# Kernel tuning notes

Measured on AMD Instinct MI355X. Metric: run time of the kernel, lower is better.

Reference implementation:

```python
import jax, jax.numpy as jnp
import numpy as np

VOCAB = 20
HID = 128
ACT = 3
IN_DIM = VOCAB + 3
NUM_GRAPHS = 64
N_P, E_P = 100000, 1600000
N_M, E_M = 50000, 800000


def _gcn_conv(x, src, dst, W, b, n_nodes):
    deg = jax.ops.segment_sum(jnp.ones(src.shape[0], x.dtype), dst, num_segments=n_nodes) + 1.0
    dinv = jax.lax.rsqrt(deg)
    xw = x @ W                                    # [N, out]
    coef = dinv[src] * dinv[dst]                  # [E]
    agg = jax.ops.segment_sum(xw[src] * coef[:, None], dst, num_segments=n_nodes)
    # self-loop contribution: norm = dinv[i]*dinv[i] = 1/deg[i]
    return agg + xw / deg[:, None] + b


def _mean_pool(x, batch, n_graphs):
    s = jax.ops.segment_sum(x, batch, num_segments=n_graphs)
    cnt = jax.ops.segment_sum(jnp.ones(x.shape[0], x.dtype), batch, num_segments=n_graphs)
    return s / jnp.maximum(cnt, 1.0)[:, None]


def setup_inputs() -> dict:
    key = jax.random.key(0)
    ks = jax.random.split(key, 24)
    d = {}
    d['residue_p'] = jax.random.randint(ks[0], (N_P,), 0, VOCAB)
    d['pos_p'] = jax.random.normal(ks[1], (N_P, 3), jnp.float32)
    d['edge_index_p'] = jax.random.randint(ks[2], (2, E_P), 0, N_P)
    d['batch_p'] = jnp.sort(jax.random.randint(ks[3], (N_P,), 0, NUM_GRAPHS))
    d['residue_m'] = jax.random.randint(ks[4], (N_M,), 0, VOCAB)
    d['pos_m'] = jax.random.normal(ks[5], (N_M, 3), jnp.float32)
    d['edge_index_m'] = jax.random.randint(ks[6], (2, E_M), 0, N_M)
    d['batch_m'] = jnp.sort(jax.random.randint(ks[7], (N_M,), 0, NUM_GRAPHS))
    s = 0.05
    d['W_p1'] = jax.random.normal(ks[8], (IN_DIM, HID), jnp.float32) * s
    d['b_p1'] = jnp.zeros((HID,), jnp.float32)
    d['W_p2'] = jax.random.normal(ks[9], (HID, HID), jnp.float32) * s
    d['b_p2'] = jnp.zeros((HID,), jnp.float32)
    d['W_m1'] = jax.random.normal(ks[10], (IN_DIM, HID), jnp.float32) * s
    d['b_m1'] = jnp.zeros((HID,), jnp.float32)
    d['W_m2'] = jax.random.normal(ks[11], (HID, HID), jnp.float32) * s
    d['b_m2'] = jnp.zeros((HID,), jnp.float32)
    d['W1'] = jax.random.normal(ks[12], (2 * HID, HID), jnp.float32) * s
    d['b1'] = jnp.zeros((HID,), jnp.float32)
    d['W2'] = jax.random.normal(ks[13], (HID, ACT), jnp.float32) * s
    d['b2'] = jnp.zeros((ACT,), jnp.float32)
    return d


def reference(residue_p, pos_p, edge_index_p, batch_p,
              residue_m, pos_m, edge_index_m, batch_m,
              W_p1, b_p1, W_p2, b_p2, W_m1, b_m1, W_m2, b_m2,
              W1, b1, W2, b2):
    # protein branch
    x_p = jnp.concatenate([jax.nn.one_hot(residue_p, VOCAB, dtype=jnp.float32), pos_p], axis=1)
    sp, dp = edge_index_p[0], edge_index_p[1]
    x_p = jax.nn.relu(_gcn_conv(x_p, sp, dp, W_p1, b_p1, N_P))
    x_p = jax.nn.relu(_gcn_conv(x_p, sp, dp, W_p2, b_p2, N_P))
    protein_embedding = _mean_pool(x_p, batch_p, NUM_GRAPHS)  # [G, HID]
    # micromolecule branch
    x_m = jnp.concatenate([jax.nn.one_hot(residue_m, VOCAB, dtype=jnp.float32), pos_m], axis=1)
    sm, dm = edge_index_m[0], edge_index_m[1]
    x_m = jax.nn.relu(_gcn_conv(x_m, sm, dm, W_m1, b_m1, N_M))
    x_m = jax.nn.relu(_gcn_conv(x_m, sm, dm, W_m2, b_m2, N_M))
    # inject protein context per micromolecule node
    ctx = protein_embedding[batch_m]                # [N_M, HID]
    feat = jnp.concatenate([x_m, ctx], axis=1)      # [N_M, 2*HID]
    h = jax.nn.relu(feat @ W1 + b1)
    return h @ W2 + b2                              # [N_M, ACT]
```

## Files before the change

kernel.cpp:

```cpp
#include <hip/hip_runtime.h>
#include <hip/hip_bf16.h>
#include <hip/hip_fp16.h>

#define HID 128
#define BIN_T 8192
#define NBMAX 1664
#define CAP 2560

typedef _Float16 f16;
typedef __attribute__((ext_vector_type(2))) _Float16 f16x2;
typedef __attribute__((ext_vector_type(4))) _Float16 f16x4;
typedef __attribute__((ext_vector_type(8))) _Float16 f16x8;
typedef __attribute__((ext_vector_type(4))) float f32x4;



__global__ void k_prep_all(const float* __restrict__ Wp2, const float* __restrict__ Wm2,
                           const float* __restrict__ W1,
                           f16* __restrict__ Wp2t, f16* __restrict__ Wm2t,
                           f16* __restrict__ W1at,
                           int* __restrict__ bcur_p, int* __restrict__ bcur_m,
                           const int* __restrict__ batch_p, int* __restrict__ pcnt,
                           float* __restrict__ psum, int N_P) {
    int idx = blockIdx.x * 256 + threadIdx.x;
    if (idx < 16384) {
        int n = idx & 127, k = idx >> 7;
        Wp2t[n * 128 + k] = (f16)Wp2[k * 128 + n];
        Wm2t[n * 128 + k] = (f16)Wm2[k * 128 + n];
        W1at[n * 128 + k] = (f16)W1[k * 128 + n];
    }
    if (idx <= NBMAX) { bcur_p[idx] = idx * CAP; bcur_m[idx] = idx * CAP; }
    if (idx < 64 * HID) psum[idx] = 0.f;
    if (idx < 64) {
        int g = idx;
        int lo = 0, hi = N_P;
        while (lo < hi) { int mid = (lo + hi) >> 1; if (batch_p[mid] < g) lo = mid + 1; else hi = mid; }
        int a = lo;
        lo = 0; hi = N_P;
        while (lo < hi) { int mid = (lo + hi) >> 1; if (batch_p[mid] < g + 1) lo = mid + 1; else hi = mid; }
        pcnt[g] = lo - a;
    }
}


__global__ void k_tile_bin2(const int* __restrict__ src_p, const int* __restrict__ dst_p,
                            int* __restrict__ bcur_p, unsigned int* __restrict__ pairs_p,
                            int E_p, int NB_p, int TP,
                            const int* __restrict__ src_m, const int* __restrict__ dst_m,
                            int* __restrict__ bcur_m, unsigned int* __restrict__ pairs_m,
                            int E_m, int NB_m) {
    __shared__ unsigned int dbuf[BIN_T];
    __shared__ unsigned short perm[BIN_T];
    __shared__ int hist[NBMAX];
    __shared__ int lbase[NBMAX];
    __shared__ int gbase[NBMAX];
    __shared__ int tt[256];
    bool isP = (int)blockIdx.x < TP;
    const int* src = isP ? src_p : src_m;
    const int* dst = isP ? dst_p : dst_m;
    int* bcursor = isP ? bcur_p : bcur_m;
    unsigned int* pairs = isP ? pairs_p : pairs_m;
    int E = isP ? E_p : E_m;
    int NB = isP ? NB_p : NB_m;
    int tilebase = (isP ? blockIdx.x : blockIdx.x - TP) * BIN_T;
    int t = threadIdx.x;
    int n = min(BIN_T, E - tilebase);
    for (int i = t; i < NB; i += 256) hist[i] = 0;
    __syncthreads();
    for (int i = t; i < n; i += 256) {
        unsigned int d = (unsigned int)dst[tilebase + i];
        dbuf[i] = d;
        atomicAdd(&hist[d >> 6], 1);
    }
    __syncthreads();
    {
        int b0 = t * 7, loc[7], run = 0;
        #pragma unroll
        for (int k = 0; k < 7; ++k) {
            int b = b0 + k;
            int c = (b < NB) ? hist[b] : 0;
            loc[k] = run; run += c;
        }
        tt[t] = run;
        __syncthreads();
        int val = run;
        for (int off = 1; off < 256; off <<= 1) {
            int add = (t >= off) ? tt[t - off] : 0;
            __syncthreads();
            tt[t] += add;
            __syncthreads();
        }
        int ebase = tt[t] - val;
        #pragma unroll
        for (int k = 0; k < 7; ++k) {
            int b = b0 + k;
            if (b < NB) lbase[b] = ebase + loc[k];
        }
    }
    __syncthreads();
    for (int i = t; i < NB; i += 256) {
        int c = hist[i];
        gbase[i] = (c > 0) ? atomicAdd(&bcursor[i], c) : 0;
    }
    __syncthreads();
    for (int i = t; i < NB; i += 256) hist[i] = lbase[i];
    __syncthreads();
    for (int i = t; i < n; i += 256) {
        int b = (int)(dbuf[i] >> 6);
        int p = atomicAdd(&hist[b], 1);
        perm[p] = (unsigned short)i;
    }
    __syncthreads();
    for (int p = t; p < n; p += 256) {
        int li = perm[p];
        unsigned int d = dbuf[li];
        int b = (int)(d >> 6);
        int addr = gbase[b] + (p - lbase[b]);
        pairs[addr] = (unsigned int)src[tilebase + li] | ((d & 63u) << 26);
    }
}


__global__ void k_fill_a(
        const unsigned int* __restrict__ pairs_p, const int* __restrict__ bcur_p,
        const int* __restrict__ res_p, const float* __restrict__ pos_p,
        int4* __restrict__ rec16_p, float* __restrict__ dinv_p,
        int* __restrict__ rowptr_p, int* __restrict__ rowend_p, int* __restrict__ csr_p,
        int N_p, int NB_p,
        const unsigned int* __restrict__ pairs_m, const int* __restrict__ bcur_m,
        const int* __restrict__ res_m, const float* __restrict__ pos_m,
        int4* __restrict__ rec16_m, float* __restrict__ dinv_m,
        int* __restrict__ rowptr_m, int* __restrict__ rowend_m, int* __restrict__ csr_m,
        int N_m) {
    __shared__ int cnt[64];
    __shared__ int cur[64];
    bool isP = (int)blockIdx.x < NB_p;
    const unsigned int* pairs = isP ? pairs_p : pairs_m;
    const int* bcur = isP ? bcur_p : bcur_m;
    const int* residue = isP ? res_p : res_m;
    const float* pos = isP ? pos_p : pos_m;
    int4* rec16 = isP ? rec16_p : rec16_m;
    float* dinvA = isP ? dinv_p : dinv_m;
    int* rowptr = isP ? rowptr_p : rowptr_m;
    int* rowend = isP ? rowend_p : rowend_m;
    int* csr_src = isP ? csr_p : csr_m;
    int N = isP ? N_p : N_m;
    int b = isP ? blockIdx.x : blockIdx.x - NB_p;
    int t = threadIdx.x, base = b * 64;
    if (t < 64) cnt[t] = 0;
    __syncthreads();
    int lo = b * CAP, hi = bcur[b];
    for (int e = lo + t; e < hi; e += 256)
        atomicAdd(&cnt[pairs[e] >> 26], 1);
    __syncthreads();
    if (t < 64) {
        int off = 0;
        for (int k = 0; k < t; ++k) off += cnt[k];
        int node = base + t;
        if (node < N) {
            rowptr[node] = lo + off;
            rowend[node] = lo + off + cnt[t];
            float d = (float)cnt[t] + 1.0f;
            float di = 1.0f / sqrtf(d);
            dinvA[node] = di;
            float px = pos[node * 3 + 0], py = pos[node * 3 + 1], pz = pos[node * 3 + 2];
            f16x4 r;
            r[0] = (f16)di; r[1] = (f16)(di * px); r[2] = (f16)(di * py); r[3] = (f16)(di * pz);
            int4 rc;
            rc.x = ((const int*)&r)[0];
            rc.y = ((const int*)&r)[1];
            rc.z = residue[node];
            rc.w = 0;
            rec16[node] = rc;
        }
        cur[t] = lo + off;
    }
    __syncthreads();
    for (int e = lo + t; e < hi; e += 256) {
        unsigned int pk = pairs[e];
        int slot = atomicAdd(&cur[pk >> 26], 1);
        csr_src[slot] = (int)(pk & 0x1FFFFu);
    }
}


__global__ __launch_bounds__(256) void k_l1(
        const unsigned int* __restrict__ pairs_p, const int* __restrict__ bcur_p,
        const int4* __restrict__ rec16_p,
        const float* __restrict__ W_p, const float* __restrict__ bias_p,
        const float* __restrict__ dinv_p, f16* __restrict__ y1_p, int N_p, int NB_p,
        const unsigned int* __restrict__ pairs_m, const int* __restrict__ bcur_m,
        const int4* __restrict__ rec16_m,
        const float* __restrict__ W_m, const float* __restrict__ bias_m,
        const float* __restrict__ dinv_m, f16* __restrict__ y1_m, int N_m) {
    __shared__ float acc[64][25];
    __shared__ float sdv[64];
    bool isP = (int)blockIdx.x < NB_p;
    const unsigned int* pairs = isP ? pairs_p : pairs_m;
    const int* bcur = isP ? bcur_p : bcur_m;
    const int4* rec16 = isP ? rec16_p : rec16_m;
    const float* W = isP ? W_p : W_m;
    const float* bias = isP ? bias_p : bias_m;
    const float* dinvA = isP ? dinv_p : dinv_m;
    f16* y1h = isP ? y1_p : y1_m;
    int N = isP ? N_p : N_m;
    int b = isP ? blockIdx.x : blockIdx.x - NB_p;
    int t = threadIdx.x, base = b * 64;
    for (int q = t; q < 64 * 25; q += 256) ((float*)acc)[q] = 0.f;
    if (t < 64 && base + t < N) sdv[t] = dinvA[base + t];
    int jj = (t & 63) * 2, slot = t >> 6;
    float wreg[23][2];
    #pragma unroll
    for (int k = 0; k < 23; ++k) {
        float2 wv = *(const float2*)&W[k * 128 + jj];
        wreg[k][0] = wv.x; wreg[k][1] = wv.y;
    }
    __syncthreads();
    int lo = b * CAP, hi = bcur[b];
    for (int e = lo + t; e < hi; e += 1024) {
        unsigned int pk[4];
        int4 rc[4];
        bool hv[4];
        #pragma unroll
        for (int u = 0; u < 4; ++u) {
            int ee = e + u * 256;
            hv[u] = ee < hi;
            pk[u] = pairs[hv[u] ? ee : e];
        }
        #pragma unroll
        for (int u = 0; u < 4; ++u)
            rc[u] = rec16[pk[u] & 0x1FFFFu];
        #pragma unroll
        for (int u = 0; u < 4; ++u) {
            if (!hv[u]) continue;
            f16x2 lo2 = *(const f16x2*)&rc[u].x;
            f16x2 hi2 = *(const f16x2*)&rc[u].y;
            int dl = (int)(pk[u] >> 26);
            int rs = rc[u].z;
            atomicAdd(&acc[dl][rs], (float)lo2[0]);
            atomicAdd(&acc[dl][20], (float)lo2[1]);
            atomicAdd(&acc[dl][21], (float)hi2[0]);
            atomicAdd(&acc[dl][22], (float)hi2[1]);
        }
    }
    __syncthreads();
    if (t < 64) {
        int node = base + t;
        if (node < N) {
            int4 rc = rec16[node];
            f16x2 lo2 = *(const f16x2*)&rc.x;
            f16x2 hi2 = *(const f16x2*)&rc.y;
            acc[t][rc.z] += (float)lo2[0];
            acc[t][20] += (float)lo2[1];
            acc[t][21] += (float)hi2[0];
            acc[t][22] += (float)hi2[1];
            float di = sdv[t];
            #pragma unroll
            for (int k = 0; k < 23; ++k) acc[t][k] *= di;
        }
    }
    __syncthreads();
    float bj0 = bias[jj], bj1 = bias[jj + 1];
    for (int r = slot * 16; r < slot * 16 + 16; ++r) {
        int node = base + r;
        if (node >= N) break;
        float a0 = bj0, a1 = bj1;
        #pragma unroll
        for (int k = 0; k < 23; ++k) {
            float zv = acc[r][k];
            a0 += zv * wreg[k][0];
            a1 += zv * wreg[k][1];
        }
        float dv = sdv[r];
        f16x2 o;
        o[0] = (f16)(fmaxf(a0, 0.f) * dv);
        o[1] = (f16)(fmaxf(a1, 0.f) * dv);
        *(f16x2*)&y1h[(size_t)node * HID + jj] = o;
    }
}


#define AGG16_TO_LDS(zs, y1h, rowptr, rowend, csr_src, dinvA, N)                \
    {                                                                           \
        const __half2* y2 = (const __half2*)y1h;                                \
        for (int i = 0; i < 4; ++i) {                                           \
            int node = tile + w * 4 + i;                                        \
            int cn = min(node, N - 1);                                          \
            int s0 = rowptr[cn], s1 = rowend[cn];                               \
            float ax = 0.f, ay = 0.f;                                           \
            int e = s0;                                                         \
            for (; e + 8 <= s1; e += 8) {                                       \
                float2 v0 = __half22float2(y2[(size_t)csr_src[e] * 64 + lane]);     \
                float2 v1 = __half22float2(y2[(size_t)csr_src[e + 1] * 64 + lane]); \
                float2 v2 = __half22float2(y2[(size_t)csr_src[e + 2] * 64 + lane]); \
                float2 v3 = __half22float2(y2[(size_t)csr_src[e + 3] * 64 + lane]); \
                float2 v4 = __half22float2(y2[(size_t)csr_src[e + 4] * 64 + lane]); \
                float2 v5 = __half22float2(y2[(size_t)csr_src[e + 5] * 64 + lane]); \
                float2 v6 = __half22float2(y2[(size_t)csr_src[e + 6] * 64 + lane]); \
                float2 v7 = __half22float2(y2[(size_t)csr_src[e + 7] * 64 + lane]); \
                ax += (v0.x + v1.x) + (v2.x + v3.x) + (v4.x + v5.x) + (v6.x + v7.x); \
                ay += (v0.y + v1.y) + (v2.y + v3.y) + (v4.y + v5.y) + (v6.y + v7.y); \
            }                                                                   \
            for (; e + 4 <= s1; e += 4) {                                       \
                float2 v0 = __half22float2(y2[(size_t)csr_src[e] * 64 + lane]);     \
                float2 v1 = __half22float2(y2[(size_t)csr_src[e + 1] * 64 + lane]); \
                float2 v2 = __half22float2(y2[(size_t)csr_src[e + 2] * 64 + lane]); \
                float2 v3 = __half22float2(y2[(size_t)csr_src[e + 3] * 64 + lane]); \
                ax += (v0.x + v1.x) + (v2.x + v3.x);                            \
                ay += (v0.y + v1.y) + (v2.y + v3.y);                            \
            }                                                                   \
            for (; e < s1; ++e) {                                               \
                float2 v = __half22float2(y2[(size_t)csr_src[e] * 64 + lane]);  \
                ax += v.x; ay += v.y;                                           \
            }                                                                   \
            float di = dinvA[cn];                                               \
            float2 vs = __half22float2(y2[(size_t)cn * 64 + lane]);             \
            f16x2 o;                                                            \
            o[0] = (f16)((ax + vs.x) * di);                                     \
            o[1] = (f16)((ay + vs.y) * di);                                     \
            *(f16x2*)&zs[w * 4 + i][lane * 2] = o;                              \
        }                                                                       \
    }                                                                           \
    __syncthreads();


__global__ __launch_bounds__(256) void k_agg_combined(
        const f16* __restrict__ y1p, const int* __restrict__ rpp, const int* __restrict__ rep,
        const int* __restrict__ csrp, const float* __restrict__ dvp,
        const f16* __restrict__ Wp2t, const float* __restrict__ bp2,
        const int* __restrict__ batchp, float* __restrict__ psum, int Np, int PB,
        const f16* __restrict__ y1m, const int* __restrict__ rpm, const int* __restrict__ rem,
        const int* __restrict__ csrm, const float* __restrict__ dvm,
        const f16* __restrict__ Wm2t, const float* __restrict__ bm2,
        f16* __restrict__ x2g, int Nm) {
    __shared__ f16 zs[16][136];
    int t = threadIdx.x, lane = t & 63, w = t >> 6;
    int lr = lane & 15, kb = lane >> 4;
    bool isP = (int)blockIdx.x < PB;
    if (isP) {
        const f16* y1h = y1p;
        int N = Np;
        int tile = blockIdx.x * 16;
        AGG16_TO_LDS(zs, y1h, rpp, rep, csrp, dvp, N)
        int g0 = batchp[min(tile, N - 1)];
        bool uni = (tile + 15 < N) && (g0 == batchp[tile + 15]);
        int gr[4]; bool val[4];
        if (!uni) {
            #pragma unroll
            for (int r = 0; r < 4; ++r) {
                int row = tile + kb * 4 + r;
                val[r] = row < N;
                gr[r] = batchp[min(row, N - 1)];
            }
        }
        f16x8 afr[4];
        #pragma unroll
        for (int kc = 0; kc < 4; ++kc)
            afr[kc] = *(const f16x8*)&zs[lr][kc * 32 + kb * 8];
        #pragma unroll
        for (int q = 0; q < 2; ++q) {
            int ct = w * 2 + q;
            f32x4 c4 = {0.f, 0.f, 0.f, 0.f};
            int col = ct * 16 + lr;
            const f16* wp = Wp2t + (size_t)col * HID + kb * 8;
            #pragma unroll
            for (int kc = 0; kc < 4; ++kc) {
                f16x8 bf = *(const f16x8*)(wp + kc * 32);
                c4 = __builtin_amdgcn_mfma_f32_16x16x32_f16(afr[kc], bf, c4, 0, 0, 0);
            }
            float bj = bp2[col];
            if (uni) {
                float ps = 0.f;
                #pragma unroll
                for (int r = 0; r < 4; ++r) ps += fmaxf(c4[r] + bj, 0.f);
                ps += __shfl_xor(ps, 16);
                ps += __shfl_xor(ps, 32);
                if (kb == 0) atomicAdd(&psum[g0 * HID + col], ps);
            } else {
                #pragma unroll
                for (int r = 0; r < 4; ++r)
                    if (val[r]) atomicAdd(&psum[gr[r] * HID + col], fmaxf(c4[r] + bj, 0.f));
            }
        }
    } else {
        const f16* y1h = y1m;
        int N = Nm;
        int tile = (blockIdx.x - PB) * 16;
        AGG16_TO_LDS(zs, y1h, rpm, rem, csrm, dvm, N)
        f16x8 afr[4];
        #pragma unroll
        for (int kc = 0; kc < 4; ++kc)
            afr[kc] = *(const f16x8*)&zs[lr][kc * 32 + kb * 8];
        __syncthreads();
        #pragma unroll
        for (int q = 0; q < 2; ++q) {
            int ct = w * 2 + q;
            f32x4 c4 = {0.f, 0.f, 0.f, 0.f};
            int col = ct * 16 + lr;
            const f16* wp = Wm2t + (size_t)col * HID + kb * 8;
            #pragma unroll
            for (int kc = 0; kc < 4; ++kc) {
                f16x8 bf = *(const f16x8*)(wp + kc * 32);
                c4 = __builtin_amdgcn_mfma_f32_16x16x32_f16(afr[kc], bf, c4, 0, 0, 0);
            }
            float bj = bm2[col];
            #pragma unroll
            for (int r = 0; r < 4; ++r)
                zs[kb * 4 + r][col] = (f16)fmaxf(c4[r] + bj, 0.f);
        }
        __syncthreads();
        int row = t >> 4, c8 = (t & 15) * 8;
        if (tile + row < N)
            *(f16x8*)&x2g[(size_t)(tile + row) * HID + c8] = *(const f16x8*)&zs[row][c8];
    }
}

__global__ void k_ctxw_div(const float* __restrict__ psum, const int* __restrict__ pcnt,
                           const float* __restrict__ W1, const float* __restrict__ b1,
                           float* __restrict__ ctxW) {
    __shared__ float pr[128];
    int g = blockIdx.x, j = threadIdx.x;
    pr[j] = psum[g * HID + j] / fmaxf((float)pcnt[g], 1.f);
    __syncthreads();
    float a = b1[j];
    #pragma unroll 4
    for (int k = 0; k < HID; ++k) a += pr[k] * W1[(HID + k) * HID + j];
    ctxW[g * HID + j] = a;
}

__global__ __launch_bounds__(256) void k_mm_finish(
        const f16* __restrict__ x2g, const int* __restrict__ batch,
        const float* __restrict__ ctxW, const f16* __restrict__ W1at,
        const float* __restrict__ W2, const float* __restrict__ b2,
        float* __restrict__ out, int N) {
    __shared__ float part[4][16][3];
    int tile = blockIdx.x * 16;
    int t = threadIdx.x, lane = t & 63, w = t >> 6;
    int lr = lane & 15, kb = lane >> 4;
    int cr = min(tile + lr, N - 1);
    f16x8 afr[4];
    #pragma unroll
    for (int kc = 0; kc < 4; ++kc)
        afr[kc] = *(const f16x8*)&x2g[(size_t)cr * HID + kc * 32 + kb * 8];
    int gidx[4];
    #pragma unroll
    for (int r = 0; r < 4; ++r)
        gidx[r] = batch[min(tile + kb * 4 + r, N - 1)];
    float po[4][3] = {};
    #pragma unroll
    for (int q = 0; q < 2; ++q) {
        int ct = w * 2 + q;
        f32x4 c4 = {0.f, 0.f, 0.f, 0.f};
        int col = ct * 16 + lr;
        const f16* wp = W1at + (size_t)col * HID + kb * 8;
        #pragma unroll
        for (int kc = 0; kc < 4; ++kc) {
            f16x8 bf = *(const f16x8*)(wp + kc * 32);
            c4 = __builtin_amdgcn_mfma_f32_16x16x32_f16(afr[kc], bf, c4, 0, 0, 0);
        }
        float w0 = W2[col * 3 + 0], w1 = W2[col * 3 + 1], w2 = W2[col * 3 + 2];
        #pragma unroll
        for (int r = 0; r < 4; ++r) {
            float h = fmaxf(c4[r] + ctxW[gidx[r] * HID + col], 0.f);
            po[r][0] += h * w0;
            po[r][1] += h * w1;
            po[r][2] += h * w2;
        }
    }
    #pragma unroll
    for (int m = 1; m < 16; m <<= 1) {
        #pragma unroll
        for (int r = 0; r < 4; ++r) {
            po[r][0] += __shfl_xor(po[r][0], m);
            po[r][1] += __shfl_xor(po[r][1], m);
            po[r][2] += __shfl_xor(po[r][2], m);
        }
    }
    if (lr == 0) {
        #pragma unroll
        for (int r = 0; r < 4; ++r) {
            part[w][kb * 4 + r][0] = po[r][0];
            part[w][kb * 4 + r][1] = po[r][1];
            part[w][kb * 4 + r][2] = po[r][2];
        }
    }
    __syncthreads();
    if (t < 48) {
        int row = t / 3, c = t - row * 3;
        int gr2 = tile + row;
        if (gr2 < N)
            out[(size_t)gr2 * 3 + c] = part[0][row][c] + part[1][row][c] +
                                       part[2][row][c] + part[3][row][c] + b2[c];
    }
}


extern "C" void kernel_launch(void* const* d_in, const int* in_sizes, int n_in,
                              void* d_out, int out_size, void* d_ws, size_t ws_size,
                              hipStream_t stream) {
    const int*   residue_p = (const int*)d_in[0];
    const float* pos_p     = (const float*)d_in[1];
    const int*   ei_p      = (const int*)d_in[2];
    const int*   batch_p   = (const int*)d_in[3];
    const int*   residue_m = (const int*)d_in[4];
    const float* pos_m     = (const float*)d_in[5];
    const int*   ei_m      = (const int*)d_in[6];
    const int*   batch_m   = (const int*)d_in[7];
    const float* W_p1 = (const float*)d_in[8];
    const float* b_p1 = (const float*)d_in[9];
    const float* W_p2 = (const float*)d_in[10];
    const float* b_p2 = (const float*)d_in[11];
    const float* W_m1 = (const float*)d_in[12];
    const float* b_m1 = (const float*)d_in[13];
    const float* W_m2 = (const float*)d_in[14];
    const float* b_m2 = (const float*)d_in[15];
    const float* W1   = (const float*)d_in[16];
    const float* b1   = (const float*)d_in[17];
    const float* W2   = (const float*)d_in[18];
    const float* b2   = (const float*)d_in[19];

    const int N_P = in_sizes[0];
    const int E_P = in_sizes[2] / 2;
    const int N_M = in_sizes[4];
    const int E_M = in_sizes[6] / 2;
    const int G = 64;
    const int NB_P = (N_P + 63) / 64;
    const int NB_M = (N_M + 63) / 64;
    const int PB = (N_P + 15) / 16;
    const int MB = (N_M + 15) / 16;

    char* ws = (char*)d_ws;
    size_t off = 0;
    auto alloc = [&](size_t bytes) {
        char* p = ws + off;
        off += (bytes + 511) & ~size_t(511);
        return p;
    };
    f16*           y1_p    = (f16*)  alloc((size_t)N_P * HID * 2);
    f16*           y1_m    = (f16*)  alloc((size_t)N_M * HID * 2);
    f16*           x2g     = (f16*)  alloc((size_t)N_M * HID * 2);
    int4*          rec16_p = (int4*) alloc((size_t)N_P * 16);
    int4*          rec16_m = (int4*) alloc((size_t)N_M * 16);
    float*         dinv_p  = (float*)alloc((size_t)N_P * 4);
    float*         dinv_m  = (float*)alloc((size_t)N_M * 4);
    int*           rp_p    = (int*)  alloc((size_t)N_P * 4);
    int*           rp_m    = (int*)  alloc((size_t)N_M * 4);
    int*           re_p    = (int*)  alloc((size_t)N_P * 4);
    int*           re_m    = (int*)  alloc((size_t)N_M * 4);
    int*           bcur_p  = (int*)  alloc((NBMAX + 1) * 4);
    int*           bcur_m  = (int*)  alloc((NBMAX + 1) * 4);
    unsigned int*  prs_p   = (unsigned int*)alloc((size_t)NB_P * CAP * 4);
    unsigned int*  prs_m   = (unsigned int*)alloc((size_t)NB_M * CAP * 4);
    int*           csr_p   = (int*)  alloc((size_t)NB_P * CAP * 4);
    int*           csr_m   = (int*)  alloc((size_t)NB_M * CAP * 4);
    float*         psum    = (float*)alloc((size_t)G * HID * 4);
    int*           pcnt    = (int*)  alloc((size_t)G * 4);
    float*         ctxW    = (float*)alloc((size_t)G * HID * 4);
    f16*           Wp2t    = (f16*)  alloc(128 * 128 * 2);
    f16*           Wm2t    = (f16*)  alloc(128 * 128 * 2);
    f16*           W1at    = (f16*)  alloc(128 * 128 * 2);

    const int TP = (E_P + BIN_T - 1) / BIN_T;
    const int TM = (E_M + BIN_T - 1) / BIN_T;

    k_prep_all<<<64, 256, 0, stream>>>(W_p2, W_m2, W1, Wp2t, Wm2t, W1at,
                                       bcur_p, bcur_m, batch_p, pcnt, psum, N_P);
    k_tile_bin2<<<TP + TM, 256, 0, stream>>>(ei_p, ei_p + E_P, bcur_p, prs_p, E_P, NB_P, TP,
                                             ei_m, ei_m + E_M, bcur_m, prs_m, E_M, NB_M);
    k_fill_a<<<NB_P + NB_M, 256, 0, stream>>>(
        prs_p, bcur_p, residue_p, pos_p, rec16_p, dinv_p, rp_p, re_p, csr_p, N_P, NB_P,
        prs_m, bcur_m, residue_m, pos_m, rec16_m, dinv_m, rp_m, re_m, csr_m, N_M);
    k_l1<<<NB_P + NB_M, 256, 0, stream>>>(
        prs_p, bcur_p, rec16_p, W_p1, b_p1, dinv_p, y1_p, N_P, NB_P,
        prs_m, bcur_m, rec16_m, W_m1, b_m1, dinv_m, y1_m, N_M);
    k_agg_combined<<<PB + MB, 256, 0, stream>>>(
        y1_p, rp_p, re_p, csr_p, dinv_p, Wp2t, b_p2, batch_p, psum, N_P, PB,
        y1_m, rp_m, re_m, csr_m, dinv_m, Wm2t, b_m2, x2g, N_M);
    k_ctxw_div<<<G, HID, 0, stream>>>(psum, pcnt, W1, b1, ctxW);
    k_mm_finish<<<MB, 256, 0, stream>>>(x2g, batch_m, ctxW, W1at, W2, b2,
                                        (float*)d_out, N_M);
}
```

Before: 278.1 us.

## Stage CSR neighbor indices in LDS and gather 16-byte rows per lane group

```diff
diff --git a/kernel.cpp b/kernel.cpp
--- a/kernel.cpp
+++ b/kernel.cpp
@@ -280,45 +280,54 @@
 }
 
 
-#define AGG16_TO_LDS(zs, y1h, rowptr, rowend, csr_src, dinvA, N)                \
+#define AGG16_TO_LDS(zs, sidx, y1h, rowptr, rowend, csr_src, dinvA, N)          \
     {                                                                           \
-        const __half2* y2 = (const __half2*)y1h;                                \
+        int sp0 = rowptr[tile];                                                 \
+        int sp1 = rowend[min(tile + 15, N - 1)];                                \
+        int slen = sp1 - sp0;                                                   \
+        for (int i = t; i < slen; i += 256) sidx[i] = csr_src[sp0 + i];         \
+        __syncthreads();                                                        \
         for (int i = 0; i < 4; ++i) {                                           \
             int node = tile + w * 4 + i;                                        \
             int cn = min(node, N - 1);                                          \
-            int s0 = rowptr[cn], s1 = rowend[cn];                               \
-            float ax = 0.f, ay = 0.f;                                           \
-            int e = s0;                                                         \
-            for (; e + 8 <= s1; e += 8) {                                       \
-                float2 v0 = __half22float2(y2[(size_t)csr_src[e] * 64 + lane]);     \
-                float2 v1 = __half22float2(y2[(size_t)csr_src[e + 1] * 64 + lane]); \
-                float2 v2 = __half22float2(y2[(size_t)csr_src[e + 2] * 64 + lane]); \
-                float2 v3 = __half22float2(y2[(size_t)csr_src[e + 3] * 64 + lane]); \
-                float2 v4 = __half22float2(y2[(size_t)csr_src[e + 4] * 64 + lane]); \
-                float2 v5 = __half22float2(y2[(size_t)csr_src[e + 5] * 64 + lane]); \
-                float2 v6 = __half22float2(y2[(size_t)csr_src[e + 6] * 64 + lane]); \
-                float2 v7 = __half22float2(y2[(size_t)csr_src[e + 7] * 64 + lane]); \
-                ax += (v0.x + v1.x) + (v2.x + v3.x) + (v4.x + v5.x) + (v6.x + v7.x); \
-                ay += (v0.y + v1.y) + (v2.y + v3.y) + (v4.y + v5.y) + (v6.y + v7.y); \
+            int lb = rowptr[cn] - sp0, le = rowend[cn] - sp0;                   \
+            float fa[8] = {};                                                   \
+            int e = lb;                                                         \
+            for (; e + 8 <= le; e += 8) {                                       \
+                int i0 = sidx[e + kb], i1 = sidx[e + 4 + kb];                   \
+                f16x8 v0 = *(const f16x8*)(y1h + (size_t)i0 * HID + lr * 8);    \
+                f16x8 v1 = *(const f16x8*)(y1h + (size_t)i1 * HID + lr * 8);    \
+                _Pragma("unroll")                                               \
+                for (int j = 0; j < 8; ++j)                                     \
+                    fa[j] += (float)v0[j] + (float)v1[j];                       \
             }                                                                   \
-            for (; e + 4 <= s1; e += 4) {                                       \
-                float2 v0 = __half22float2(y2[(size_t)csr_src[e] * 64 + lane]);     \
-                float2 v1 = __half22float2(y2[(size_t)csr_src[e + 1] * 64 + lane]); \
-                float2 v2 = __half22float2(y2[(size_t)csr_src[e + 2] * 64 + lane]); \
-                float2 v3 = __half22float2(y2[(size_t)csr_src[e + 3] * 64 + lane]); \
-                ax += (v0.x + v1.x) + (v2.x + v3.x);                            \
-                ay += (v0.y + v1.y) + (v2.y + v3.y);                            \
+            if (e + 4 <= le) {                                                  \
+                int i0 = sidx[e + kb];                                          \
+                f16x8 v0 = *(const f16x8*)(y1h + (size_t)i0 * HID + lr * 8);    \
+                _Pragma("unroll")                                               \
+                for (int j = 0; j < 8; ++j) fa[j] += (float)v0[j];              \
+                e += 4;                                                         \
             }                                                                   \
-            for (; e < s1; ++e) {                                               \
-                float2 v = __half22float2(y2[(size_t)csr_src[e] * 64 + lane]);  \
-                ax += v.x; ay += v.y;                                           \
+            if (e + kb < le) {                                                  \
+                int i0 = sidx[e + kb];                                          \
+                f16x8 v0 = *(const f16x8*)(y1h + (size_t)i0 * HID + lr * 8);    \
+                _Pragma("unroll")                                               \
+                for (int j = 0; j < 8; ++j) fa[j] += (float)v0[j];              \
             }                                                                   \
-            float di = dinvA[cn];                                               \
-            float2 vs = __half22float2(y2[(size_t)cn * 64 + lane]);             \
-            f16x2 o;                                                            \
-            o[0] = (f16)((ax + vs.x) * di);                                     \
-            o[1] = (f16)((ay + vs.y) * di);                                     \
-            *(f16x2*)&zs[w * 4 + i][lane * 2] = o;                              \
+            _Pragma("unroll")                                                   \
+            for (int j = 0; j < 8; ++j) {                                       \
+                fa[j] += __shfl_xor(fa[j], 16);                                 \
+                fa[j] += __shfl_xor(fa[j], 32);                                 \
+            }                                                                   \
+            if (kb == 0) {                                                      \
+                f16x8 sv = *(const f16x8*)(y1h + (size_t)cn * HID + lr * 8);    \
+                float di = dinvA[cn];                                           \
+                f16x8 o;                                                        \
+                _Pragma("unroll")                                               \
+                for (int j = 0; j < 8; ++j)                                     \
+                    o[j] = (f16)((fa[j] + (float)sv[j]) * di);                  \
+                *(f16x8*)&zs[w * 4 + i][lr * 8] = o;                            \
+            }                                                                   \
         }                                                                       \
     }                                                                           \
     __syncthreads();
@@ -333,7 +342,8 @@
         const int* __restrict__ csrm, const float* __restrict__ dvm,
         const f16* __restrict__ Wm2t, const float* __restrict__ bm2,
         f16* __restrict__ x2g, int Nm) {
-    __shared__ f16 zs[16][136];
+    __shared__ __attribute__((aligned(16))) f16 zs[16][136];
+    __shared__ int sidx[CAP];
     int t = threadIdx.x, lane = t & 63, w = t >> 6;
     int lr = lane & 15, kb = lane >> 4;
     bool isP = (int)blockIdx.x < PB;
@@ -341,7 +351,7 @@
         const f16* y1h = y1p;
         int N = Np;
         int tile = blockIdx.x * 16;
-        AGG16_TO_LDS(zs, y1h, rpp, rep, csrp, dvp, N)
+        AGG16_TO_LDS(zs, sidx, y1h, rpp, rep, csrp, dvp, N)
         int g0 = batchp[min(tile, N - 1)];
         bool uni = (tile + 15 < N) && (g0 == batchp[tile + 15]);
         int gr[4]; bool val[4];
@@ -386,7 +396,7 @@
         const f16* y1h = y1m;
         int N = Nm;
         int tile = (blockIdx.x - PB) * 16;
-        AGG16_TO_LDS(zs, y1h, rpm, rem, csrm, dvm, N)
+        AGG16_TO_LDS(zs, sidx, y1h, rpm, rem, csrm, dvm, N)
         f16x8 afr[4];
         #pragma unroll
         for (int kc = 0; kc < 4; ++kc)
```

Result: faster. 270.0 us (-2.9%).
